# Kernel optimization log

Measured on AMD Instinct MI355X. Metric: run time of the kernel, lower is better.

## Reference

```python
import jax, jax.numpy as jnp
import numpy as np

FEAT_DIM = 256
DEPTH = 2
N = 8192


def setup_inputs() -> dict:
    key = jax.random.key(0)
    ks = jax.random.split(key, 5)
    bd = 1.0 / FEAT_DIM
    X = jax.random.normal(ks[0], (N, FEAT_DIM), dtype=jnp.float32)
    coefs = jax.random.normal(ks[1], (N,), dtype=jnp.float32)
    linear = jax.random.uniform(ks[2], (DEPTH, FEAT_DIM), minval=-bd, maxval=bd, dtype=jnp.float32)
    dirv = jax.random.uniform(ks[3], (DEPTH, FEAT_DIM), minval=-bd, maxval=bd, dtype=jnp.float32)
    feat = jax.random.uniform(ks[4], (DEPTH, FEAT_DIM), minval=-bd, maxval=bd, dtype=jnp.float32)
    return {"X": X, "coefs": coefs, "linear": linear, "dirv": dirv, "feat": feat}


def reference(X, coefs, linear, dirv, feat):
    # coefs is unused: the torch forward returns before the coef_embed branch.
    emb = X
    n = X.shape[0]
    for i in range(linear.shape[0]):  # depth: small fixed loop
        # torch: emb3[j,a,k] = linear[a]*emb[j,k]; q = sum_a feat[a]*emb3 = (feat.linear)*emb
        a = jnp.dot(feat[i], linear[i])
        b = jnp.dot(dirv[i], linear[i])
        q = a * emb                      # [N, F]
        k = b * emb                      # [N, F]
        k_norm = k / jnp.linalg.norm(k)  # global Frobenius norm, as torch.norm(k)
        inner = jnp.sum(q * k_norm, axis=-1)            # [N]
        scale = jnp.where(inner <= 0, inner, 0.0)       # inner * (inner<=0)
        emb = q - scale[:, None] * k_norm
        # graph_block: X_up[i] = X[i] + (X@X[i]) @ (X - X[i]) / N
        # == X + (S@X - rowsum(S)*X)/N with S = X X^T
        S = emb @ emb.T                                 # [N, N]
        emb = emb + (S @ emb - jnp.sum(S, axis=1, keepdims=True) * emb) / n
    out = jnp.mean(emb @ emb.T, axis=-1)[:-1]           # [N-1]
    return out
```

## Files before the change

kernel.cpp:

```cpp
#include <hip/hip_runtime.h>
#include <math.h>

constexpr int NROW = 8192;
constexpr int FD   = 256;

typedef unsigned short u16;
typedef __attribute__((ext_vector_type(8))) short short8;
typedef __attribute__((ext_vector_type(4))) float f32x4;


__device__ __forceinline__ float f_of(float nj, float A, float B, float AB) {
    float inner = AB * nj;
    return A - (inner <= 0.f ? inner : 0.f) * B;
}
__device__ __forceinline__ float wred(float s) {
    #pragma unroll
    for (int off = 32; off; off >>= 1) s += __shfl_xor(s, off);
    return s;
}
__device__ __forceinline__ float dot4(float4 a, float4 b) {
    return a.x*b.x + a.y*b.y + a.z*b.z + a.w*b.w;
}
__device__ __forceinline__ u16 f2bf(float x) {
    unsigned int u = __float_as_uint(x);
    u = (u + 0x7FFFu + ((u >> 16) & 1u)) >> 16;
    return (u16)u;
}

__global__ void k_norm(const float* __restrict__ in, float* __restrict__ nrm,
                       float* __restrict__ fpart) {
    __shared__ float bs[4];
    int wave = threadIdx.x >> 6, lane = threadIdx.x & 63;
    int row = blockIdx.x * 4 + wave;
    const float4 v = *(const float4*)&in[(size_t)row * FD + lane * 4];
    float s = wred(dot4(v, v));
    if (lane == 0) { nrm[row] = s; bs[wave] = s; }
    __syncthreads();
    if (threadIdx.x == 0) fpart[blockIdx.x] = bs[0] + bs[1] + bs[2] + bs[3];
}

__global__ void k_red(const float* __restrict__ fpart, int n, float* __restrict__ scal,
                      const float* __restrict__ linear, const float* __restrict__ dirv,
                      const float* __restrict__ feat) {
    __shared__ float l[256];
    int tid = threadIdx.x;
    if (tid < 64) {
        for (int i = 0; i < 2; ++i) {
            float pa = 0.f, pb = 0.f;
            for (int k = tid; k < FD; k += 64) {
                float ll = linear[i*FD + k];
                pa += feat[i*FD + k] * ll;
                pb += dirv[i*FD + k] * ll;
            }
            pa = wred(pa); pb = wred(pb);
            if (tid == 0) { scal[i] = pa; scal[2 + i] = pb; }
        }
    }
    float s = 0.f;
    for (int j = tid; j < n; j += 256) s += fpart[j];
    l[tid] = s;
    __syncthreads();
    for (int off = 128; off; off >>= 1) {
        if (tid < off) l[tid] += l[tid + off];
        __syncthreads();
    }
    if (tid == 0) {
        float F2 = l[0];
        float a = scal[0], b = scal[2];
        float sb = (b > 0.f) ? 1.f : ((b < 0.f) ? -1.f : 0.f);
        float B = sb / sqrtf(F2);
        scal[4] = a; scal[5] = B; scal[6] = a * B; scal[7] = F2;
    }
}

__global__ void __launch_bounds__(256, 2)
k_prep(const float* __restrict__ X, const float* __restrict__ nrm0,
       const float* __restrict__ scal, u16* __restrict__ Rbf,
       u16* __restrict__ Rt, float* __restrict__ cpart) {
    __shared__ u16 Ltr[256][72];
    __shared__ float cred[4][256];
    __shared__ float ff[64];
    const int tid = threadIdx.x;
    const int r0 = blockIdx.x * 64;
    if (tid < 64) ff[tid] = f_of(nrm0[r0 + tid], scal[4], scal[5], scal[6]);
    __syncthreads();
    const int cg = (tid & 63) * 4;
    const int rg = tid >> 6;
    float4 csum = make_float4(0.f, 0.f, 0.f, 0.f);
    for (int i = 0; i < 16; ++i) {
        int row = rg * 16 + i;
        float4 v = *(const float4*)&X[(size_t)(r0 + row) * FD + cg];
        float f = ff[row];
        v.x *= f; v.y *= f; v.z *= f; v.w *= f;
        csum.x += v.x; csum.y += v.y; csum.z += v.z; csum.w += v.w;
        u16 h0 = f2bf(v.x), h1 = f2bf(v.y), h2 = f2bf(v.z), h3 = f2bf(v.w);
        u16* rb = Rbf + (size_t)(r0 + row) * FD + cg;
        rb[0] = h0; rb[1] = h1; rb[2] = h2; rb[3] = h3;
        Ltr[cg + 0][row] = h0; Ltr[cg + 1][row] = h1;
        Ltr[cg + 2][row] = h2; Ltr[cg + 3][row] = h3;
    }
    *(float4*)&cred[rg][cg] = csum;
    __syncthreads();
    cpart[(size_t)blockIdx.x * FD + tid] =
        cred[0][tid] + cred[1][tid] + cred[2][tid] + cred[3][tid];
    #pragma unroll
    for (int it = 0; it < 4; ++it) {
        int c = (tid >> 2) + it * 64;
        int chunk = (tid & 3) * 16;
        uint4 u0 = *(const uint4*)&Ltr[c][chunk];
        uint4 u1 = *(const uint4*)&Ltr[c][chunk + 8];
        u16* rt = Rt + (size_t)c * NROW + r0 + chunk;
        *(uint4*)(rt)     = u0;
        *(uint4*)(rt + 8) = u1;
    }
}

__global__ void __launch_bounds__(256, 2)
k_gram(const u16* __restrict__ Rt, float* __restrict__ Gp) {
    const int bi = blockIdx.x, bj = blockIdx.y, z = blockIdx.z;
    const int tid = threadIdx.x, w = tid >> 6, lane = tid & 63;
    const int l15 = lane & 15, quad = lane >> 4;
    const int m0 = bi * 64 + (w & 1) * 32;
    const int n0 = bj * 64 + (w >> 1) * 32;
    const size_t kbase = (size_t)z * 256 + quad * 8;
    const u16* am0 = Rt + (size_t)(m0 + l15) * NROW + kbase;
    const u16* am1 = am0 + (size_t)16 * NROW;
    const u16* bn0 = Rt + (size_t)(n0 + l15) * NROW + kbase;
    const u16* bn1 = bn0 + (size_t)16 * NROW;
    f32x4 acc[2][2] = {};
    #pragma unroll
    for (int s = 0; s < 8; ++s) {
        int ko = s * 32;
        short8 a0 = *(const short8*)(am0 + ko);
        short8 a1 = *(const short8*)(am1 + ko);
        short8 b0 = *(const short8*)(bn0 + ko);
        short8 b1 = *(const short8*)(bn1 + ko);
        acc[0][0] = __builtin_amdgcn_mfma_f32_16x16x32_bf16(a0, b0, acc[0][0], 0, 0, 0);
        acc[0][1] = __builtin_amdgcn_mfma_f32_16x16x32_bf16(a0, b1, acc[0][1], 0, 0, 0);
        acc[1][0] = __builtin_amdgcn_mfma_f32_16x16x32_bf16(a1, b0, acc[1][0], 0, 0, 0);
        acc[1][1] = __builtin_amdgcn_mfma_f32_16x16x32_bf16(a1, b1, acc[1][1], 0, 0, 0);
    }
    float* gz = Gp + (size_t)z * (FD * FD);
    #pragma unroll
    for (int mi = 0; mi < 2; ++mi)
        #pragma unroll
        for (int ni = 0; ni < 2; ++ni)
            #pragma unroll
            for (int r = 0; r < 4; ++r)
                gz[(size_t)(m0 + mi*16 + quad*4 + r) * FD + n0 + ni*16 + l15] =
                    acc[mi][ni][r];
}

__global__ void k_gred(const float* __restrict__ Gp, const float* __restrict__ cpart,
                       u16* __restrict__ Gbf, float* __restrict__ c0) {
    int tid = threadIdx.x;
    if (blockIdx.x < 256) {
        size_t e0 = (size_t)blockIdx.x * 256 + tid;
        float s = 0.f;
        #pragma unroll 8
        for (int z = 0; z < 32; ++z) s += Gp[(size_t)z * (FD * FD) + e0];
        Gbf[e0] = f2bf(s);
    } else {
        float s = 0.f;
        #pragma unroll 8
        for (int b = 0; b < 128; ++b) s += cpart[(size_t)b * FD + tid];
        c0[tid] = s;
    }
}

__global__ void __launch_bounds__(256, 2)
k_apply(const float* __restrict__ X, const u16* __restrict__ Rbf,
        const u16* __restrict__ Gbf, const float* __restrict__ nrm0,
        const float* __restrict__ scal, const float* __restrict__ c0,
        float* __restrict__ emb, float* __restrict__ nrm1,
        float* __restrict__ fpart1, float* __restrict__ cpart1,
        float* __restrict__ wpart1) {
    __shared__ float Sl[32][260];
    __shared__ float u0s[32], ffs[32], nrs[32];
    __shared__ float nw[32][4];
    const int tid = threadIdx.x, w = tid >> 6, lane = tid & 63;
    const int l15 = lane & 15, quad = lane >> 4;
    const int r0 = blockIdx.x * 32;
    const float A = scal[4], B = scal[5], AB = scal[6];

    if (tid < 32) ffs[tid] = f_of(nrm0[r0 + tid], A, B, AB);
    __syncthreads();
    #pragma unroll
    for (int jj = 0; jj < 8; ++jj) {
        int row = w * 8 + jj;
        float4 xv = *(const float4*)&X[(size_t)(r0 + row) * FD + lane * 4];
        float4 cv = *(const float4*)&c0[lane * 4];
        float t = wred(dot4(xv, cv));
        if (lane == 0) u0s[row] = ffs[row] * t;
    }

    const u16* ap0 = Rbf + (size_t)(r0 + l15) * FD + quad * 8;
    const u16* ap1 = ap0 + (size_t)16 * FD;
    const int n0w = w * 64;
    const u16* bp = Gbf + (size_t)(n0w + l15) * FD + quad * 8;
    f32x4 acc[2][4] = {};
    #pragma unroll
    for (int s = 0; s < 8; ++s) {
        int ko = s * 32;
        short8 a0 = *(const short8*)(ap0 + ko);
        short8 a1 = *(const short8*)(ap1 + ko);
        short8 b0 = *(const short8*)(bp + ko);
        short8 b1 = *(const short8*)(bp + 16 * FD + ko);
        short8 b2 = *(const short8*)(bp + 32 * FD + ko);
        short8 b3 = *(const short8*)(bp + 48 * FD + ko);
        acc[0][0] = __builtin_amdgcn_mfma_f32_16x16x32_bf16(a0, b0, acc[0][0], 0, 0, 0);
        acc[0][1] = __builtin_amdgcn_mfma_f32_16x16x32_bf16(a0, b1, acc[0][1], 0, 0, 0);
        acc[0][2] = __builtin_amdgcn_mfma_f32_16x16x32_bf16(a0, b2, acc[0][2], 0, 0, 0);
        acc[0][3] = __builtin_amdgcn_mfma_f32_16x16x32_bf16(a0, b3, acc[0][3], 0, 0, 0);
        acc[1][0] = __builtin_amdgcn_mfma_f32_16x16x32_bf16(a1, b0, acc[1][0], 0, 0, 0);
        acc[1][1] = __builtin_amdgcn_mfma_f32_16x16x32_bf16(a1, b1, acc[1][1], 0, 0, 0);
        acc[1][2] = __builtin_amdgcn_mfma_f32_16x16x32_bf16(a1, b2, acc[1][2], 0, 0, 0);
        acc[1][3] = __builtin_amdgcn_mfma_f32_16x16x32_bf16(a1, b3, acc[1][3], 0, 0, 0);
    }
    #pragma unroll
    for (int mi = 0; mi < 2; ++mi)
        #pragma unroll
        for (int ni = 0; ni < 4; ++ni)
            #pragma unroll
            for (int r = 0; r < 4; ++r)
                Sl[mi*16 + quad*4 + r][n0w + ni*16 + l15] = acc[mi][ni][r];
    __syncthreads();

    const float invN = 1.0f / NROW;
    float er[32];
    float csum = 0.f;
    #pragma unroll
    for (int j = 0; j < 32; ++j) {
        float x = X[(size_t)(r0 + j) * FD + tid];
        float rv = ffs[j] * x;
        float e = rv + (Sl[j][tid] - u0s[j] * rv) * invN;
        emb[(size_t)(r0 + j) * FD + tid] = e;
        er[j] = e;
        csum += e;
        float s2 = wred(e * e);
        if (lane == 0) nw[j][w] = s2;
    }
    __syncthreads();
    if (tid < 32) {
        float nn = nw[tid][0] + nw[tid][1] + nw[tid][2] + nw[tid][3];
        nrm1[r0 + tid] = nn;
        nrs[tid] = nn;
    }
    __syncthreads();
    float wsum = 0.f;
    #pragma unroll
    for (int j = 0; j < 32; ++j) wsum += nrs[j] * er[j];
    cpart1[(size_t)blockIdx.x * FD + tid] = csum;
    wpart1[(size_t)blockIdx.x * FD + tid] = wsum;
    if (tid == 0) {
        float fp = 0.f;
        #pragma unroll
        for (int j = 0; j < 32; ++j) fp += nrs[j];
        fpart1[blockIdx.x] = fp;
    }
}

__device__ __forceinline__ void red1_scal(const float* fpart1, const float* scal,
                                          float* l, float& A, float& B, float& AB,
                                          float& kap) {
    int tid = threadIdx.x;
    l[tid] = fpart1[tid];
    __syncthreads();
    for (int off = 128; off; off >>= 1) {
        if (tid < off) l[tid] += l[tid + off];
        __syncthreads();
    }
    float F2 = l[0];
    float a = scal[1], b = scal[3];
    float sb = (b > 0.f) ? 1.f : ((b < 0.f) ? -1.f : 0.f);
    B = sb / sqrtf(F2);
    A = a; AB = a * B;
    kap = (AB <= 0.f) ? AB * B : 0.f;
    __syncthreads();
}

__global__ void k_sv(const float* __restrict__ fpart1, const float* __restrict__ scal,
                     const float* __restrict__ cpart1, const float* __restrict__ wpart1,
                     float* __restrict__ svec) {
    __shared__ float l[256];
    float A1, B1, AB1, kap;
    red1_scal(fpart1, scal, l, A1, B1, AB1, kap);
    int tid = threadIdx.x;
    int col = blockIdx.x * 4 + (tid >> 6);
    int lane = tid & 63;
    float cs = 0.f, wsm = 0.f;
    #pragma unroll
    for (int b = lane; b < 256; b += 64) {
        cs  += cpart1[(size_t)b * FD + col];
        wsm += wpart1[(size_t)b * FD + col];
    }
    #pragma unroll
    for (int off = 32; off; off >>= 1) {
        cs  += __shfl_down(cs, off);
        wsm += __shfl_down(wsm, off);
    }
    if (lane == 0) svec[col] = A1 * cs - kap * wsm;
}

__global__ void k_uv(const float* __restrict__ emb, const float* __restrict__ nrm1,
                     const float* __restrict__ scal, const float* __restrict__ fpart1,
                     const float* __restrict__ svec, float* __restrict__ u,
                     float* __restrict__ vpart) {
    __shared__ float l[256];
    __shared__ float ssh[FD];
    __shared__ float uf[16];
    float A, B, AB, kap;
    red1_scal(fpart1, scal, l, A, B, AB, kap);
    int tid = threadIdx.x;
    int r0 = blockIdx.x * 16;
    ssh[tid] = svec[tid];
    __syncthreads();
    const int wave = tid >> 6, lane = tid & 63;
    float4 sv = *(const float4*)&ssh[lane*4];
    #pragma unroll
    for (int jj = 0; jj < 4; ++jj) {
        int row = r0 + wave * 4 + jj;
        float4 ev = *(const float4*)&emb[(size_t)row * FD + lane*4];
        float s = wred(dot4(ev, sv));
        if (lane == 0) {
            float f = A - kap * nrm1[row];
            float uj = f * s;
            u[row] = uj;
            uf[wave*4 + jj] = uj * f;
        }
    }
    __syncthreads();
    float vp = 0.f;
    #pragma unroll
    for (int j = 0; j < 16; ++j)
        vp += uf[j] * emb[(size_t)(r0 + j) * FD + tid];
    vpart[(size_t)blockIdx.x * FD + tid] = vp;
}

__global__ void k_vred(const float* __restrict__ part, float* __restrict__ vec) {
    int tid = threadIdx.x;
    int col = blockIdx.x * 4 + (tid >> 6);
    int lane = tid & 63;
    float s = 0.f;
    #pragma unroll
    for (int b = 0; b < 8; ++b) s += part[(size_t)(b * 64 + lane) * FD + col];
    #pragma unroll
    for (int off = 32; off; off >>= 1) s += __shfl_down(s, off);
    if (lane == 0) vec[col] = s;
}

__global__ void k_out(const float* __restrict__ emb, const float* __restrict__ nrm1,
                      const float* __restrict__ scal, const float* __restrict__ fpart1,
                      const float* __restrict__ vvec, const float* __restrict__ u,
                      float* __restrict__ out) {
    __shared__ float l[256];
    __shared__ float vsh[FD];
    float A, B, AB, kap;
    red1_scal(fpart1, scal, l, A, B, AB, kap);
    int tid = threadIdx.x;
    int r0 = blockIdx.x * 16;
    vsh[tid] = vvec[tid];
    __syncthreads();
    const int wave = tid >> 6, lane = tid & 63;
    const float invN = 1.0f / NROW;
    float4 vv = *(const float4*)&vsh[lane*4];
    #pragma unroll
    for (int jj = 0; jj < 4; ++jj) {
        int row = r0 + wave * 4 + jj;
        float4 ev = *(const float4*)&emb[(size_t)row * FD + lane*4];
        float s = wred(dot4(ev, vv));
        if (lane == 0 && row < NROW - 1) {
            float f = A - kap * nrm1[row];
            float uj = u[row];
            out[row] = (uj + (f * s - uj * uj) * invN) * invN;
        }
    }
}

extern "C" void kernel_launch(void* const* d_in, const int* in_sizes, int n_in,
                              void* d_out, int out_size, void* d_ws, size_t ws_size,
                              hipStream_t stream) {
    const float* X      = (const float*)d_in[0];
    const float* linear = (const float*)d_in[2];
    const float* dirv   = (const float*)d_in[3];
    const float* feat   = (const float*)d_in[4];
    float* out = (float*)d_out;

    char* ws = (char*)d_ws;
    float* scal   = (float*)(ws + 0);
    float* nrm0   = (float*)(ws + 4096);
    float* nrm1   = (float*)(ws + 36864);
    float* fpart  = (float*)(ws + 69632);
    float* fpart1 = (float*)(ws + 77824);
    float* c0     = (float*)(ws + 78848);
    float* svec   = (float*)(ws + 79872);
    float* vvec   = (float*)(ws + 80896);
    float* u      = (float*)(ws + 81920);
    float* cpart  = (float*)(ws + 114688);
    u16*   Gbf    = (u16*)  (ws + 245760);
    float* cpart1 = (float*)(ws + 376832);
    float* wpart1 = (float*)(ws + 638976);
    float* vpart  = (float*)(ws + 895232);
    u16*   Rbf    = (u16*)  (ws + 2097152);
    u16*   Rt     = (u16*)  (ws + 6291456);
    float* Gp     = (float*)(ws + 10485760);
    float* emb    = (float*)(ws + 18874368);

    k_norm<<<NROW/4, 256, 0, stream>>>(X, nrm0, fpart);
    k_red<<<1, 256, 0, stream>>>(fpart, 2048, scal, linear, dirv, feat);
    k_prep<<<128, 256, 0, stream>>>(X, nrm0, scal, Rbf, Rt, cpart);
    k_gram<<<dim3(4,4,32), 256, 0, stream>>>(Rt, Gp);
    k_gred<<<257, 256, 0, stream>>>(Gp, cpart, Gbf, c0);
    k_apply<<<256, 256, 0, stream>>>(X, Rbf, Gbf, nrm0, scal, c0, emb, nrm1,
                                     fpart1, cpart1, wpart1);
    k_sv<<<64, 256, 0, stream>>>(fpart1, scal, cpart1, wpart1, svec);
    k_uv<<<NROW/16, 256, 0, stream>>>(emb, nrm1, scal, fpart1, svec, u, vpart);
    k_vred<<<64, 256, 0, stream>>>(vpart, vvec);
    k_out<<<NROW/16, 256, 0, stream>>>(emb, nrm1, scal, fpart1, vvec, u, out);
}
```

Before: 136.0 us.

## Fuse scalar reduction into prep, halve gram split-K, rework transpose and norm reduction

Removes the single-block k_red launch by having every k_prep block redundantly reduce fpart and compute the scalar coefficients, with block 0 writing scal. The per-row factor f is now stored once to f0 and read by k_apply instead of being recomputed. The LDS transpose now uses a row-major tile with packed stores, and the gram split-K goes from 32 to 16 slices with double the K per block, which halves the partial-sum traffic in k_gred but gives fewer blocks. k_apply also replaces per-row wave shuffles with an LDS-based row-norm reduction.

New measurement: 127.1 us. 6.5% less time.

```diff
diff --git a/kernel.cpp b/kernel.cpp
--- a/kernel.cpp
+++ b/kernel.cpp
@@ -3,6 +3,7 @@
 
 constexpr int NROW = 8192;
 constexpr int FD   = 256;
+constexpr int NZ   = 16;
 
 typedef unsigned short u16;
 typedef __attribute__((ext_vector_type(8))) short short8;
@@ -39,11 +40,20 @@
     if (threadIdx.x == 0) fpart[blockIdx.x] = bs[0] + bs[1] + bs[2] + bs[3];
 }
 
-__global__ void k_red(const float* __restrict__ fpart, int n, float* __restrict__ scal,
-                      const float* __restrict__ linear, const float* __restrict__ dirv,
-                      const float* __restrict__ feat) {
+__global__ void __launch_bounds__(256, 2)
+k_prep(const float* __restrict__ X, const float* __restrict__ nrm0,
+       const float* __restrict__ fpart, const float* __restrict__ linear,
+       const float* __restrict__ dirv, const float* __restrict__ feat,
+       float* __restrict__ scal, float* __restrict__ f0,
+       u16* __restrict__ Rbf, u16* __restrict__ Rt, float* __restrict__ cpart) {
+    __shared__ u16 T[64][264];
+    __shared__ float cred[4][256];
     __shared__ float l[256];
-    int tid = threadIdx.x;
+    __shared__ float ff[64];
+    __shared__ float sdot[4];
+    const int tid = threadIdx.x;
+    const int r0 = blockIdx.x * 64;
+
     if (tid < 64) {
         for (int i = 0; i < 2; ++i) {
             float pa = 0.f, pb = 0.f;
@@ -53,37 +63,34 @@
                 pb += dirv[i*FD + k] * ll;
             }
             pa = wred(pa); pb = wred(pb);
-            if (tid == 0) { scal[i] = pa; scal[2 + i] = pb; }
+            if (tid == 0) { sdot[i] = pa; sdot[2 + i] = pb; }
         }
     }
     float s = 0.f;
-    for (int j = tid; j < n; j += 256) s += fpart[j];
+    #pragma unroll
+    for (int k = 0; k < 8; ++k) s += fpart[tid + k * 256];
     l[tid] = s;
     __syncthreads();
     for (int off = 128; off; off >>= 1) {
         if (tid < off) l[tid] += l[tid + off];
         __syncthreads();
     }
-    if (tid == 0) {
-        float F2 = l[0];
-        float a = scal[0], b = scal[2];
-        float sb = (b > 0.f) ? 1.f : ((b < 0.f) ? -1.f : 0.f);
-        float B = sb / sqrtf(F2);
-        scal[4] = a; scal[5] = B; scal[6] = a * B; scal[7] = F2;
-    }
-}
-
-__global__ void __launch_bounds__(256, 2)
-k_prep(const float* __restrict__ X, const float* __restrict__ nrm0,
-       const float* __restrict__ scal, u16* __restrict__ Rbf,
-       u16* __restrict__ Rt, float* __restrict__ cpart) {
-    __shared__ u16 Ltr[256][72];
-    __shared__ float cred[4][256];
-    __shared__ float ff[64];
-    const int tid = threadIdx.x;
-    const int r0 = blockIdx.x * 64;
-    if (tid < 64) ff[tid] = f_of(nrm0[r0 + tid], scal[4], scal[5], scal[6]);
-    __syncthreads();
+    const float F2 = l[0];
+    const float a = sdot[0], b = sdot[2];
+    const float sb = (b > 0.f) ? 1.f : ((b < 0.f) ? -1.f : 0.f);
+    const float B = sb / sqrtf(F2);
+    const float A = a, AB = a * B;
+    if (blockIdx.x == 0 && tid == 0) {
+        scal[0] = sdot[0]; scal[1] = sdot[1]; scal[2] = sdot[2]; scal[3] = sdot[3];
+        scal[4] = A; scal[5] = B; scal[6] = AB; scal[7] = F2;
+    }
+    if (tid < 64) {
+        float f = f_of(nrm0[r0 + tid], A, B, AB);
+        ff[tid] = f;
+        f0[r0 + tid] = f;
+    }
+    __syncthreads();
+
     const int cg = (tid & 63) * 4;
     const int rg = tid >> 6;
     float4 csum = make_float4(0.f, 0.f, 0.f, 0.f);
@@ -93,25 +100,26 @@
         float f = ff[row];
         v.x *= f; v.y *= f; v.z *= f; v.w *= f;
         csum.x += v.x; csum.y += v.y; csum.z += v.z; csum.w += v.w;
-        u16 h0 = f2bf(v.x), h1 = f2bf(v.y), h2 = f2bf(v.z), h3 = f2bf(v.w);
-        u16* rb = Rbf + (size_t)(r0 + row) * FD + cg;
-        rb[0] = h0; rb[1] = h1; rb[2] = h2; rb[3] = h3;
-        Ltr[cg + 0][row] = h0; Ltr[cg + 1][row] = h1;
-        Ltr[cg + 2][row] = h2; Ltr[cg + 3][row] = h3;
+        unsigned lo = (unsigned)f2bf(v.x) | ((unsigned)f2bf(v.y) << 16);
+        unsigned hi = (unsigned)f2bf(v.z) | ((unsigned)f2bf(v.w) << 16);
+        uint2 pk = make_uint2(lo, hi);
+        *(uint2*)&Rbf[(size_t)(r0 + row) * FD + cg] = pk;
+        *(uint2*)&T[row][cg] = pk;
     }
     *(float4*)&cred[rg][cg] = csum;
     __syncthreads();
     cpart[(size_t)blockIdx.x * FD + tid] =
         cred[0][tid] + cred[1][tid] + cred[2][tid] + cred[3][tid];
-    #pragma unroll
-    for (int it = 0; it < 4; ++it) {
-        int c = (tid >> 2) + it * 64;
-        int chunk = (tid & 3) * 16;
-        uint4 u0 = *(const uint4*)&Ltr[c][chunk];
-        uint4 u1 = *(const uint4*)&Ltr[c][chunk + 8];
-        u16* rt = Rt + (size_t)c * NROW + r0 + chunk;
-        *(uint4*)(rt)     = u0;
-        *(uint4*)(rt + 8) = u1;
+
+    const int c = tid;
+    #pragma unroll
+    for (int ch = 0; ch < 8; ++ch) {
+        unsigned w0 = (unsigned)T[ch*8+0][c] | ((unsigned)T[ch*8+1][c] << 16);
+        unsigned w1 = (unsigned)T[ch*8+2][c] | ((unsigned)T[ch*8+3][c] << 16);
+        unsigned w2 = (unsigned)T[ch*8+4][c] | ((unsigned)T[ch*8+5][c] << 16);
+        unsigned w3 = (unsigned)T[ch*8+6][c] | ((unsigned)T[ch*8+7][c] << 16);
+        uint4 o = make_uint4(w0, w1, w2, w3);
+        *(uint4*)&Rt[(size_t)c * NROW + r0 + ch * 8] = o;
     }
 }
 
@@ -122,14 +130,14 @@
     const int l15 = lane & 15, quad = lane >> 4;
     const int m0 = bi * 64 + (w & 1) * 32;
     const int n0 = bj * 64 + (w >> 1) * 32;
-    const size_t kbase = (size_t)z * 256 + quad * 8;
+    const size_t kbase = (size_t)z * 512 + quad * 8;
     const u16* am0 = Rt + (size_t)(m0 + l15) * NROW + kbase;
     const u16* am1 = am0 + (size_t)16 * NROW;
     const u16* bn0 = Rt + (size_t)(n0 + l15) * NROW + kbase;
     const u16* bn1 = bn0 + (size_t)16 * NROW;
     f32x4 acc[2][2] = {};
     #pragma unroll
-    for (int s = 0; s < 8; ++s) {
+    for (int s = 0; s < 16; ++s) {
         int ko = s * 32;
         short8 a0 = *(const short8*)(am0 + ko);
         short8 a1 = *(const short8*)(am1 + ko);
@@ -157,8 +165,8 @@
     if (blockIdx.x < 256) {
         size_t e0 = (size_t)blockIdx.x * 256 + tid;
         float s = 0.f;
-        #pragma unroll 8
-        for (int z = 0; z < 32; ++z) s += Gp[(size_t)z * (FD * FD) + e0];
+        #pragma unroll
+        for (int z = 0; z < NZ; ++z) s += Gp[(size_t)z * (FD * FD) + e0];
         Gbf[e0] = f2bf(s);
     } else {
         float s = 0.f;
@@ -170,20 +178,18 @@
 
 __global__ void __launch_bounds__(256, 2)
 k_apply(const float* __restrict__ X, const u16* __restrict__ Rbf,
-        const u16* __restrict__ Gbf, const float* __restrict__ nrm0,
-        const float* __restrict__ scal, const float* __restrict__ c0,
-        float* __restrict__ emb, float* __restrict__ nrm1,
-        float* __restrict__ fpart1, float* __restrict__ cpart1,
-        float* __restrict__ wpart1) {
+        const u16* __restrict__ Gbf, const float* __restrict__ f0,
+        const float* __restrict__ c0, float* __restrict__ emb,
+        float* __restrict__ nrm1, float* __restrict__ fpart1,
+        float* __restrict__ cpart1, float* __restrict__ wpart1) {
     __shared__ float Sl[32][260];
     __shared__ float u0s[32], ffs[32], nrs[32];
-    __shared__ float nw[32][4];
+    __shared__ float nw8[32][8];
     const int tid = threadIdx.x, w = tid >> 6, lane = tid & 63;
     const int l15 = lane & 15, quad = lane >> 4;
     const int r0 = blockIdx.x * 32;
-    const float A = scal[4], B = scal[5], AB = scal[6];
-
-    if (tid < 32) ffs[tid] = f_of(nrm0[r0 + tid], A, B, AB);
+
+    if (tid < 32) ffs[tid] = f0[r0 + tid];
     __syncthreads();
     #pragma unroll
     for (int jj = 0; jj < 8; ++jj) {
@@ -237,12 +243,21 @@
         emb[(size_t)(r0 + j) * FD + tid] = e;
         er[j] = e;
         csum += e;
-        float s2 = wred(e * e);
-        if (lane == 0) nw[j][w] = s2;
+        Sl[j][tid] = e * e;
+    }
+    __syncthreads();
+    {
+        int row = tid & 31, q = tid >> 5;
+        float pn = 0.f;
+        #pragma unroll
+        for (int i = 0; i < 32; ++i) pn += Sl[row][q * 32 + i];
+        nw8[row][q] = pn;
     }
     __syncthreads();
     if (tid < 32) {
-        float nn = nw[tid][0] + nw[tid][1] + nw[tid][2] + nw[tid][3];
+        float nn = 0.f;
+        #pragma unroll
+        for (int q = 0; q < 8; ++q) nn += nw8[tid][q];
         nrm1[r0 + tid] = nn;
         nrs[tid] = nn;
     }
@@ -396,22 +411,23 @@
     float* svec   = (float*)(ws + 79872);
     float* vvec   = (float*)(ws + 80896);
     float* u      = (float*)(ws + 81920);
-    float* cpart  = (float*)(ws + 114688);
-    u16*   Gbf    = (u16*)  (ws + 245760);
-    float* cpart1 = (float*)(ws + 376832);
-    float* wpart1 = (float*)(ws + 638976);
-    float* vpart  = (float*)(ws + 895232);
+    float* f0     = (float*)(ws + 114688);
+    float* cpart  = (float*)(ws + 147456);
+    u16*   Gbf    = (u16*)  (ws + 278528);
+    float* cpart1 = (float*)(ws + 409600);
+    float* wpart1 = (float*)(ws + 671744);
+    float* vpart  = (float*)(ws + 933888);
     u16*   Rbf    = (u16*)  (ws + 2097152);
     u16*   Rt     = (u16*)  (ws + 6291456);
     float* Gp     = (float*)(ws + 10485760);
     float* emb    = (float*)(ws + 18874368);
 
     k_norm<<<NROW/4, 256, 0, stream>>>(X, nrm0, fpart);
-    k_red<<<1, 256, 0, stream>>>(fpart, 2048, scal, linear, dirv, feat);
-    k_prep<<<128, 256, 0, stream>>>(X, nrm0, scal, Rbf, Rt, cpart);
-    k_gram<<<dim3(4,4,32), 256, 0, stream>>>(Rt, Gp);
+    k_prep<<<128, 256, 0, stream>>>(X, nrm0, fpart, linear, dirv, feat,
+                                    scal, f0, Rbf, Rt, cpart);
+    k_gram<<<dim3(4,4,NZ), 256, 0, stream>>>(Rt, Gp);
     k_gred<<<257, 256, 0, stream>>>(Gp, cpart, Gbf, c0);
-    k_apply<<<256, 256, 0, stream>>>(X, Rbf, Gbf, nrm0, scal, c0, emb, nrm1,
+    k_apply<<<256, 256, 0, stream>>>(X, Rbf, Gbf, f0, c0, emb, nrm1,
                                      fpart1, cpart1, wpart1);
     k_sv<<<64, 256, 0, stream>>>(fpart1, scal, cpart1, wpart1, svec);
     k_uv<<<NROW/16, 256, 0, stream>>>(emb, nrm1, scal, fpart1, svec, u, vpart);
```
